# Optimization experiments

Hardware: AMD Instinct MI355X
Metric: run time of the kernel (lower is better)

## Reference

```python
import jax, jax.numpy as jnp
import numpy as np

# ---- static hash-grid config (instant-NGP style, matches tcnn hash.json) ----
N_LEVELS = 16
F_PER_LEVEL = 2
LOG2_T = 19
TABLE_SIZE = 2 ** LOG2_T          # 524288 entries per level
BASE_RES = 16
PER_LEVEL_SCALE = 1.3819          # finest res ~2048
RES = [int(np.floor(BASE_RES * PER_LEVEL_SCALE ** l)) for l in range(N_LEVELS)]
N_POINTS = 2 ** 21
PRIME_Y = np.uint32(2654435761)   # tcnn spatial-hash prime

_CORNERS = jnp.array([[0, 0], [1, 0], [0, 1], [1, 1]], dtype=jnp.uint32)


def _level_features(x, table, res):
    """Bilinear hash-grid lookup for one level. x: [N,2] in [0,1). -> [N,F]."""
    pos = x * res                      # [N,2]
    x0f = jnp.floor(pos)
    w = pos - x0f                      # interpolation fractions [N,2]
    x0 = x0f.astype(jnp.uint32)
    c = x0[:, None, :] + _CORNERS[None]            # [N,4,2] corner coords
    if (res + 1) ** 2 <= TABLE_SIZE:
        # dense grid fits in the table: linear indexing (as tcnn does)
        idx = c[..., 0] + c[..., 1] * jnp.uint32(res + 1)
    else:
        # spatial hash with uint32 wraparound
        idx = (c[..., 0] ^ (c[..., 1] * PRIME_Y)) & jnp.uint32(TABLE_SIZE - 1)
    feats = table[idx.astype(jnp.int32)]           # [N,4,F] irregular gather
    wx = jnp.where(_CORNERS[None, :, 0] == 1, w[:, None, 0], 1.0 - w[:, None, 0])
    wy = jnp.where(_CORNERS[None, :, 1] == 1, w[:, None, 1], 1.0 - w[:, None, 1])
    return jnp.sum(feats * (wx * wy)[..., None], axis=1)  # [N,F]


def setup_inputs() -> dict:
    key = jax.random.key(0)
    k1, k2, k3, k4, k5 = jax.random.split(key, 5)
    x = jax.random.uniform(k1, (N_POINTS, 2), dtype=jnp.float32)
    # tcnn hash tables are initialized uniform in [-1e-4, 1e-4]
    tables = jax.random.uniform(k2, (N_LEVELS, TABLE_SIZE, F_PER_LEVEL),
                                dtype=jnp.float32, minval=-1e-4, maxval=1e-4)
    d_in = 2 + N_LEVELS * F_PER_LEVEL  # 34
    h = 64
    w1 = jax.random.normal(k3, (d_in, h), dtype=jnp.float32) * (1.0 / np.sqrt(d_in))
    w2 = jax.random.normal(k4, (h, h), dtype=jnp.float32) * (1.0 / np.sqrt(h))
    w3 = jax.random.normal(k5, (h, 3), dtype=jnp.float32) * (1.0 / np.sqrt(h))
    return {"x": x, "tables": tables, "w1": w1, "w2": w2, "w3": w3}


def reference(x, tables, w1, w2, w3):
    # multi-res hash grid encode (16 levels, static small loop)
    feats = [_level_features(x, tables[l], RES[l]) for l in range(N_LEVELS)]
    enc = jnp.concatenate([x] + feats, axis=1)     # [N, 2 + 32]
    # tiny fused MLP decode (no biases, as in tcnn networks)
    h = jax.nn.relu(enc @ w1)
    h = jax.nn.relu(h @ w2)
    return h @ w3                                   # [N, 3]
```

## Files before the change

kernel.cpp:

```cpp
#include <hip/hip_runtime.h>

typedef unsigned int u32;
typedef unsigned short u16;
typedef __attribute__((ext_vector_type(8))) short s16x8;
typedef __attribute__((ext_vector_type(4))) float f32x4;
typedef float f32x4a __attribute__((ext_vector_type(4), aligned(8)));
typedef u32  u32x2a  __attribute__((ext_vector_type(2), aligned(4)));

#define TBL    524288u
#define TMASK  (TBL - 1u)
#define HPRIME 2654435761u

__device__ constexpr int RESI[16] = {16,22,30,42,58,80,111,153,212,294,406,561,775,1072,1481,2047};

static __device__ __forceinline__ u16 f2bf(float f){
  u32 u = __builtin_bit_cast(u32, f);
  return (u16)((u + 0x7fffu + ((u >> 16) & 1u)) >> 16);
}
static __device__ __forceinline__ float bf2f(u16 h){ return __builtin_bit_cast(float, (u32)h << 16); }
static __device__ __forceinline__ float blo(u32 e){ return __builtin_bit_cast(float, (u32)(e << 16)); }
static __device__ __forceinline__ float bhi(u32 e){ return __builtin_bit_cast(float, (u32)(e & 0xffff0000u)); }
static __device__ __forceinline__ u32 packbf2(float a, float b){ return (u32)f2bf(a) | ((u32)f2bf(b) << 16); }
static __device__ __forceinline__ u32 cvtpk(float a, float b){
  u32 r; asm("v_cvt_pk_bf16_f32 %0, %1, %2" : "=v"(r) : "v"(a), "v"(b)); return r;
}

#define MFMA(A,B,C) __builtin_amdgcn_mfma_f32_16x16x32_bf16((A),(B),(C),0,0,0)

__global__ __launch_bounds__(256) void cvt_tab(const float4* __restrict__ src,
                                               uint2* __restrict__ dst, int n4) {
  for (int i = blockIdx.x*256 + threadIdx.x; i < n4; i += gridDim.x*256) {
    const float4 v = src[i];
    dst[i] = make_uint2(packbf2(v.x, v.y), packbf2(v.z, v.w));
  }
}

template<bool PACKED>
__global__ __launch_bounds__(256, 2) void ngp_fused(
    const float2* __restrict__ xq,
    const float2* __restrict__ tab32,
    const u32*    __restrict__ ctab,
    const float*  __restrict__ w1,
    const float*  __restrict__ w2,
    const float*  __restrict__ w3,
    float* __restrict__ out,
    int iters)
{
  __shared__ __align__(16) u16   encS[256 * 40];
  __shared__ __align__(16) float xyS [256 * 2];
  __shared__ __align__(16) u16   hS  [4][2][16*80];
  __shared__ __align__(16) s16x8 wS  [10][64];

  const int tid  = threadIdx.x;
  const int lane = tid & 63;
  const int wv   = tid >> 6;
  const int m    = lane & 15;
  const int q    = lane >> 4;

  float w1x[4], w1y[4];
  s16x8 B1[4], B2h[4][2], B3h[2];
  #pragma unroll
  for (int c = 0; c < 4; ++c) {
    const int n = c*16 + m;
    w1x[c] = w1[n]; w1y[c] = w1[64 + n];
    s16x8 f1;
    #pragma unroll
    for (int j = 0; j < 8; ++j) {
      const int k = q*8 + j;
      f1[j] = (short)f2bf(w1[(2 + k)*64 + n]);
    }
    B1[c] = f1;
    #pragma unroll
    for (int s = 0; s < 2; ++s) {
      s16x8 fh, fl;
      #pragma unroll
      for (int j = 0; j < 8; ++j) {
        const int k = s*32 + q*8 + j;
        const float v = w2[k*64 + n];
        const u16 h = f2bf(v);
        fh[j] = (short)h; fl[j] = (short)f2bf(v - bf2f(h));
      }
      B2h[c][s] = fh;
      if (wv == 0) wS[c*2 + s][lane] = fl;
    }
  }
  #pragma unroll
  for (int s = 0; s < 2; ++s) {
    s16x8 fh, fl;
    #pragma unroll
    for (int j = 0; j < 8; ++j) {
      const int k = s*32 + q*8 + j;
      const float v = (m < 3) ? w3[k*3 + m] : 0.f;
      const u16 h = f2bf(v);
      fh[j] = (short)h; fl[j] = (short)f2bf(v - bf2f(h));
    }
    B3h[s] = fh;
    if (wv == 0) wS[8 + s][lane] = fl;
  }
  __syncthreads();

  u16* const hpl = &hS[wv][0][0];
  u16* const lpl = &hS[wv][1][0];

  for (int it = 0; it < iters; ++it) {
    const int base = (blockIdx.x * iters + it) << 8;

    {
      const float2 xy = xq[base + tid];
      ((float2*)xyS)[tid] = xy;
      const float xf = xy.x, yf = xy.y;
      u32 er[16];
      #pragma unroll
      for (int l = 0; l < 16; ++l) {
        const int res = RESI[l];
        const float px = xf * (float)res, py = yf * (float)res;
        const float fx = floorf(px), fy = floorf(py);
        const float wx = px - fx, wy = py - fy;
        const u32 ix = (u32)fx, iy = (u32)fy;
        const float w00 = (1.f-wx)*(1.f-wy), w10 = wx*(1.f-wy);
        const float w01 = (1.f-wx)*wy,       w11 = wx*wy;
        float f0, f1;
        if (l < 12) {
          const u32 st  = (u32)res + 1u;
          const u32 i00 = ix + iy*st;
          if (PACKED) {
            const u32* t = ctab + (size_t)l * TBL;
            const u32x2a eA = *(const u32x2a*)&t[i00];
            const u32x2a eB = *(const u32x2a*)&t[i00 + st];
            f0 = blo(eA[0])*w00 + blo(eA[1])*w10 + blo(eB[0])*w01 + blo(eB[1])*w11;
            f1 = bhi(eA[0])*w00 + bhi(eA[1])*w10 + bhi(eB[0])*w01 + bhi(eB[1])*w11;
          } else {
            const float2* t = tab32 + (size_t)l * TBL;
            const f32x4a eA = *(const f32x4a*)&t[i00];
            const f32x4a eB = *(const f32x4a*)&t[i00 + st];
            f0 = eA[0]*w00 + eA[2]*w10 + eB[0]*w01 + eB[2]*w11;
            f1 = eA[1]*w00 + eA[3]*w10 + eB[1]*w01 + eB[3]*w11;
          }
        } else {
          const u32 hy = iy * HPRIME, hy1 = hy + HPRIME;
          const u32 i00 = ( ix        ^ hy ) & TMASK;
          const u32 i10 = ((ix + 1u)  ^ hy ) & TMASK;
          const u32 i01 = ( ix        ^ hy1) & TMASK;
          const u32 i11 = ((ix + 1u)  ^ hy1) & TMASK;
          if (PACKED) {
            const u32* t = ctab + (size_t)l * TBL;
            const u32 e00 = t[i00], e10 = t[i10], e01 = t[i01], e11 = t[i11];
            f0 = blo(e00)*w00 + blo(e10)*w10 + blo(e01)*w01 + blo(e11)*w11;
            f1 = bhi(e00)*w00 + bhi(e10)*w10 + bhi(e01)*w01 + bhi(e11)*w11;
          } else {
            const float2* t = tab32 + (size_t)l * TBL;
            const float2 e00 = t[i00], e10 = t[i10], e01 = t[i01], e11 = t[i11];
            f0 = e00.x*w00 + e10.x*w10 + e01.x*w01 + e11.x*w11;
            f1 = e00.y*w00 + e10.y*w10 + e01.y*w01 + e11.y*w11;
          }
        }
        er[l] = cvtpk(f0, f1);
      }
      uint4* rowp = (uint4*)&encS[tid * 40];
      rowp[0] = make_uint4(er[0],  er[1],  er[2],  er[3]);
      rowp[1] = make_uint4(er[4],  er[5],  er[6],  er[7]);
      rowp[2] = make_uint4(er[8],  er[9],  er[10], er[11]);
      rowp[3] = make_uint4(er[12], er[13], er[14], er[15]);
    }

    #pragma unroll 1
    for (int t4 = 0; t4 < 4; ++t4) {
      const int rbase = wv*64 + t4*16;
      const s16x8 a1 = *(const s16x8*)&encS[(rbase + m)*40 + q*8];

      float xr[4], yr[4];
      #pragma unroll
      for (int r = 0; r < 4; ++r) {
        const float2 v = ((const float2*)xyS)[rbase + q*4 + r];
        xr[r] = v.x; yr[r] = v.y;
      }

      f32x4 acc[4];
      #pragma unroll
      for (int c = 0; c < 4; ++c) {
        f32x4 z;
        #pragma unroll
        for (int r = 0; r < 4; ++r) z[r] = xr[r]*w1x[c] + yr[r]*w1y[c];
        acc[c] = MFMA(a1, B1[c], z);
      }

      #pragma unroll
      for (int c = 0; c < 4; ++c)
        #pragma unroll
        for (int r = 0; r < 4; ++r) {
          const float h = fmaxf(acc[c][r], 0.f);
          const u32 hp_ = cvtpk(h, h);
          const float lf = h - __builtin_bit_cast(float, hp_ << 16);
          const u32 lp_ = cvtpk(lf, lf);
          const int idx = (q*4 + r)*80 + c*16 + m;
          hpl[idx] = (u16)hp_;
          lpl[idx] = (u16)lp_;
        }

      s16x8 hi0 = *(const s16x8*)&hpl[m*80 + q*8];
      s16x8 hi1 = *(const s16x8*)&hpl[m*80 + 32 + q*8];
      s16x8 lo0 = *(const s16x8*)&lpl[m*80 + q*8];
      s16x8 lo1 = *(const s16x8*)&lpl[m*80 + 32 + q*8];

      #pragma unroll
      for (int c = 0; c < 4; ++c) {
        const s16x8 b2l0 = wS[c*2 + 0][lane];
        const s16x8 b2l1 = wS[c*2 + 1][lane];
        f32x4 z = {0.f,0.f,0.f,0.f};
        z = MFMA(hi0, B2h[c][0], z); z = MFMA(hi1, B2h[c][1], z);
        z = MFMA(lo0, B2h[c][0], z); z = MFMA(lo1, B2h[c][1], z);
        z = MFMA(hi0, b2l0,      z); z = MFMA(hi1, b2l1,      z);
        acc[c] = z;
      }

      #pragma unroll
      for (int c = 0; c < 4; ++c)
        #pragma unroll
        for (int r = 0; r < 4; ++r) {
          const float h = fmaxf(acc[c][r], 0.f);
          const u32 hp_ = cvtpk(h, h);
          const float lf = h - __builtin_bit_cast(float, hp_ << 16);
          const u32 lp_ = cvtpk(lf, lf);
          const int idx = (q*4 + r)*80 + c*16 + m;
          hpl[idx] = (u16)hp_;
          lpl[idx] = (u16)lp_;
        }

      hi0 = *(const s16x8*)&hpl[m*80 + q*8];
      hi1 = *(const s16x8*)&hpl[m*80 + 32 + q*8];
      lo0 = *(const s16x8*)&lpl[m*80 + q*8];
      lo1 = *(const s16x8*)&lpl[m*80 + 32 + q*8];

      const s16x8 b3l0 = wS[8][lane];
      const s16x8 b3l1 = wS[9][lane];
      f32x4 z = {0.f,0.f,0.f,0.f};
      z = MFMA(hi0, B3h[0], z); z = MFMA(hi1, B3h[1], z);
      z = MFMA(lo0, B3h[0], z); z = MFMA(lo1, B3h[1], z);
      z = MFMA(hi0, b3l0,   z); z = MFMA(hi1, b3l1,   z);

      if (m < 3) {
        #pragma unroll
        for (int r = 0; r < 4; ++r)
          out[(size_t)(base + rbase + q*4 + r)*3 + m] = z[r];
      }
    }
  }
}

extern "C" void kernel_launch(void* const* d_in, const int* in_sizes, int n_in,
                              void* d_out, int out_size, void* d_ws, size_t ws_size,
                              hipStream_t stream) {
  const int N = in_sizes[0] / 2;
  const int ITERS = 4;
  const int blocks = N / (256 * ITERS);
  const size_t ctab_bytes = (size_t)16 * TBL * 4;
  if (ws_size >= ctab_bytes) {
    cvt_tab<<<2048, 256, 0, stream>>>((const float4*)d_in[1], (uint2*)d_ws, (int)(16*TBL/2));
    ngp_fused<true><<<blocks, 256, 0, stream>>>(
        (const float2*)d_in[0], (const float2*)d_in[1], (const u32*)d_ws,
        (const float*)d_in[2], (const float*)d_in[3], (const float*)d_in[4],
        (float*)d_out, ITERS);
  } else {
    ngp_fused<false><<<blocks, 256, 0, stream>>>(
        (const float2*)d_in[0], (const float2*)d_in[1], (const u32*)d_ws,
        (const float*)d_in[2], (const float*)d_in[3], (const float*)d_in[4],
        (float*)d_out, ITERS);
  }
}
```

Baseline: 458.4 us.

## Issue hashed-level gathers first and XOR-swizzle hidden activation LDS layout

```diff
diff --git a/kernel.cpp b/kernel.cpp
--- a/kernel.cpp
+++ b/kernel.cpp
@@ -101,6 +101,7 @@
 
   u16* const hpl = &hS[wv][0][0];
   u16* const lpl = &hS[wv][1][0];
+  const int mq8  = (m & 12) << 1;
 
   for (int it = 0; it < iters; ++it) {
     const int base = (blockIdx.x * iters + it) << 8;
@@ -110,51 +111,83 @@
       ((float2*)xyS)[tid] = xy;
       const float xf = xy.x, yf = xy.y;
       u32 er[16];
-      #pragma unroll
-      for (int l = 0; l < 16; ++l) {
-        const int res = RESI[l];
-        const float px = xf * (float)res, py = yf * (float)res;
-        const float fx = floorf(px), fy = floorf(py);
-        const float wx = px - fx, wy = py - fy;
-        const u32 ix = (u32)fx, iy = (u32)fy;
-        const float w00 = (1.f-wx)*(1.f-wy), w10 = wx*(1.f-wy);
-        const float w01 = (1.f-wx)*wy,       w11 = wx*wy;
-        float f0, f1;
-        if (l < 12) {
+      if constexpr (PACKED) {
+        u32 hv[4][4];
+        #pragma unroll
+        for (int l = 12; l < 16; ++l) {
+          const int res = RESI[l];
+          const u32 ix = (u32)floorf(xf * (float)res);
+          const u32 iy = (u32)floorf(yf * (float)res);
+          const u32 hy = iy * HPRIME, hy1 = hy + HPRIME;
+          const u32* t = ctab + (size_t)l * TBL;
+          hv[l-12][0] = t[( ix       ^ hy ) & TMASK];
+          hv[l-12][1] = t[((ix + 1u) ^ hy ) & TMASK];
+          hv[l-12][2] = t[( ix       ^ hy1) & TMASK];
+          hv[l-12][3] = t[((ix + 1u) ^ hy1) & TMASK];
+        }
+        #pragma unroll
+        for (int l = 0; l < 12; ++l) {
+          const int res = RESI[l];
+          const float px = xf * (float)res, py = yf * (float)res;
+          const float fx = floorf(px), fy = floorf(py);
+          const float wx = px - fx, wy = py - fy;
+          const u32 ix = (u32)fx, iy = (u32)fy;
+          const float w00 = (1.f-wx)*(1.f-wy), w10 = wx*(1.f-wy);
+          const float w01 = (1.f-wx)*wy,       w11 = wx*wy;
           const u32 st  = (u32)res + 1u;
           const u32 i00 = ix + iy*st;
-          if (PACKED) {
-            const u32* t = ctab + (size_t)l * TBL;
-            const u32x2a eA = *(const u32x2a*)&t[i00];
-            const u32x2a eB = *(const u32x2a*)&t[i00 + st];
-            f0 = blo(eA[0])*w00 + blo(eA[1])*w10 + blo(eB[0])*w01 + blo(eB[1])*w11;
-            f1 = bhi(eA[0])*w00 + bhi(eA[1])*w10 + bhi(eB[0])*w01 + bhi(eB[1])*w11;
-          } else {
+          const u32* t = ctab + (size_t)l * TBL;
+          const u32x2a eA = *(const u32x2a*)&t[i00];
+          const u32x2a eB = *(const u32x2a*)&t[i00 + st];
+          const float f0 = blo(eA[0])*w00 + blo(eA[1])*w10 + blo(eB[0])*w01 + blo(eB[1])*w11;
+          const float f1 = bhi(eA[0])*w00 + bhi(eA[1])*w10 + bhi(eB[0])*w01 + bhi(eB[1])*w11;
+          er[l] = cvtpk(f0, f1);
+        }
+        #pragma unroll
+        for (int hl = 0; hl < 4; ++hl) {
+          const int res = RESI[12 + hl];
+          const float px = xf * (float)res, py = yf * (float)res;
+          const float wx = px - floorf(px), wy = py - floorf(py);
+          const float w00 = (1.f-wx)*(1.f-wy), w10 = wx*(1.f-wy);
+          const float w01 = (1.f-wx)*wy,       w11 = wx*wy;
+          const float f0 = blo(hv[hl][0])*w00 + blo(hv[hl][1])*w10
+                         + blo(hv[hl][2])*w01 + blo(hv[hl][3])*w11;
+          const float f1 = bhi(hv[hl][0])*w00 + bhi(hv[hl][1])*w10
+                         + bhi(hv[hl][2])*w01 + bhi(hv[hl][3])*w11;
+          er[12 + hl] = cvtpk(f0, f1);
+        }
+      } else {
+        #pragma unroll
+        for (int l = 0; l < 16; ++l) {
+          const int res = RESI[l];
+          const float px = xf * (float)res, py = yf * (float)res;
+          const float fx = floorf(px), fy = floorf(py);
+          const float wx = px - fx, wy = py - fy;
+          const u32 ix = (u32)fx, iy = (u32)fy;
+          const float w00 = (1.f-wx)*(1.f-wy), w10 = wx*(1.f-wy);
+          const float w01 = (1.f-wx)*wy,       w11 = wx*wy;
+          float f0, f1;
+          if (l < 12) {
+            const u32 st  = (u32)res + 1u;
+            const u32 i00 = ix + iy*st;
             const float2* t = tab32 + (size_t)l * TBL;
             const f32x4a eA = *(const f32x4a*)&t[i00];
             const f32x4a eB = *(const f32x4a*)&t[i00 + st];
             f0 = eA[0]*w00 + eA[2]*w10 + eB[0]*w01 + eB[2]*w11;
             f1 = eA[1]*w00 + eA[3]*w10 + eB[1]*w01 + eB[3]*w11;
-          }
-        } else {
-          const u32 hy = iy * HPRIME, hy1 = hy + HPRIME;
-          const u32 i00 = ( ix        ^ hy ) & TMASK;
-          const u32 i10 = ((ix + 1u)  ^ hy ) & TMASK;
-          const u32 i01 = ( ix        ^ hy1) & TMASK;
-          const u32 i11 = ((ix + 1u)  ^ hy1) & TMASK;
-          if (PACKED) {
-            const u32* t = ctab + (size_t)l * TBL;
-            const u32 e00 = t[i00], e10 = t[i10], e01 = t[i01], e11 = t[i11];
-            f0 = blo(e00)*w00 + blo(e10)*w10 + blo(e01)*w01 + blo(e11)*w11;
-            f1 = bhi(e00)*w00 + bhi(e10)*w10 + bhi(e01)*w01 + bhi(e11)*w11;
           } else {
+            const u32 hy = iy * HPRIME, hy1 = hy + HPRIME;
+            const u32 i00 = ( ix        ^ hy ) & TMASK;
+            const u32 i10 = ((ix + 1u)  ^ hy ) & TMASK;
+            const u32 i01 = ( ix        ^ hy1) & TMASK;
+            const u32 i11 = ((ix + 1u)  ^ hy1) & TMASK;
             const float2* t = tab32 + (size_t)l * TBL;
             const float2 e00 = t[i00], e10 = t[i10], e01 = t[i01], e11 = t[i11];
             f0 = e00.x*w00 + e10.x*w10 + e01.x*w01 + e11.x*w11;
             f1 = e00.y*w00 + e10.y*w10 + e01.y*w01 + e11.y*w11;
           }
-        }
-        er[l] = cvtpk(f0, f1);
+          er[l] = cvtpk(f0, f1);
+        }
       }
       uint4* rowp = (uint4*)&encS[tid * 40];
       rowp[0] = make_uint4(er[0],  er[1],  er[2],  er[3]);
@@ -192,15 +225,15 @@
           const u32 hp_ = cvtpk(h, h);
           const float lf = h - __builtin_bit_cast(float, hp_ << 16);
           const u32 lp_ = cvtpk(lf, lf);
-          const int idx = (q*4 + r)*80 + c*16 + m;
+          const int idx = (q*4 + r)*80 + ((c*16 + m) ^ (q << 3));
           hpl[idx] = (u16)hp_;
           lpl[idx] = (u16)lp_;
         }
 
-      s16x8 hi0 = *(const s16x8*)&hpl[m*80 + q*8];
-      s16x8 hi1 = *(const s16x8*)&hpl[m*80 + 32 + q*8];
-      s16x8 lo0 = *(const s16x8*)&lpl[m*80 + q*8];
-      s16x8 lo1 = *(const s16x8*)&lpl[m*80 + 32 + q*8];
+      s16x8 hi0 = *(const s16x8*)&hpl[m*80 + ((q*8) ^ mq8)];
+      s16x8 hi1 = *(const s16x8*)&hpl[m*80 + 32 + ((q*8) ^ mq8)];
+      s16x8 lo0 = *(const s16x8*)&lpl[m*80 + ((q*8) ^ mq8)];
+      s16x8 lo1 = *(const s16x8*)&lpl[m*80 + 32 + ((q*8) ^ mq8)];
 
       #pragma unroll
       for (int c = 0; c < 4; ++c) {
@@ -221,15 +254,15 @@
           const u32 hp_ = cvtpk(h, h);
           const float lf = h - __builtin_bit_cast(float, hp_ << 16);
           const u32 lp_ = cvtpk(lf, lf);
-          const int idx = (q*4 + r)*80 + c*16 + m;
+          const int idx = (q*4 + r)*80 + ((c*16 + m) ^ (q << 3));
           hpl[idx] = (u16)hp_;
           lpl[idx] = (u16)lp_;
         }
 
-      hi0 = *(const s16x8*)&hpl[m*80 + q*8];
-      hi1 = *(const s16x8*)&hpl[m*80 + 32 + q*8];
-      lo0 = *(const s16x8*)&lpl[m*80 + q*8];
-      lo1 = *(const s16x8*)&lpl[m*80 + 32 + q*8];
+      hi0 = *(const s16x8*)&hpl[m*80 + ((q*8) ^ mq8)];
+      hi1 = *(const s16x8*)&hpl[m*80 + 32 + ((q*8) ^ mq8)];
+      lo0 = *(const s16x8*)&lpl[m*80 + ((q*8) ^ mq8)];
+      lo1 = *(const s16x8*)&lpl[m*80 + 32 + ((q*8) ^ mq8)];
 
       const s16x8 b3l0 = wS[8][lane];
       const s16x8 b3l1 = wS[9][lane];
```

Result: faster. 433.7 us (-5.4%).
